# Optimization experiments

Hardware: AMD Instinct MI355X
Metric: run time of the kernel (lower is better)

The kernel has to match this reference:

```python
import jax, jax.numpy as jnp
import numpy as np

B, T, S = 4, 64, 256
E_ENC = 512   # encoder_hidden_size
D_DEC = 512   # decoder_hidden_size (must equal E_ENC per original math)
F_EMB = 128   # field_embed_size


def setup_inputs() -> dict:
    key = jax.random.key(0)
    ks = jax.random.split(key, 11)
    s = 0.05
    return {
        "output": jax.random.normal(ks[0], (B, T, D_DEC), jnp.float32),
        "encoder_hidden": jax.random.normal(ks[1], (S, B, E_ENC), jnp.float32),
        "input_z": jax.random.normal(ks[2], (B, S, F_EMB), jnp.float32),
        "W1": jax.random.normal(ks[3], (D_DEC, E_ENC), jnp.float32) * s,
        "b1": jnp.zeros((D_DEC,), jnp.float32),
        "W2": jax.random.normal(ks[4], (D_DEC, D_DEC), jnp.float32) * s,
        "b2": jnp.zeros((D_DEC,), jnp.float32),
        "W3": jax.random.normal(ks[5], (D_DEC, F_EMB), jnp.float32) * s,
        "b3": jnp.zeros((D_DEC,), jnp.float32),
        "W4": jax.random.normal(ks[6], (D_DEC, D_DEC), jnp.float32) * s,
        "b4": jnp.zeros((D_DEC,), jnp.float32),
    }


def reference(output, encoder_hidden, input_z, W1, b1, W2, b2, W3, b3, W4, b4):
    # out_hs: tanh(lin1(encoder_hidden)) on [S,B,D], then .view -> reshape to [B,S,D]
    out_hs = jnp.tanh(jnp.einsum('sbe,de->sbd', encoder_hidden, W1) + b1)
    out_hs = out_hs.reshape(out_hs.shape[1], out_hs.shape[0], out_hs.shape[2])  # [B,S,D] (raw view, as in torch)
    enc_r = encoder_hidden.reshape(encoder_hidden.shape[1], encoder_hidden.shape[0], encoder_hidden.shape[2])  # [B,S,E]

    out_fds = jnp.tanh(jnp.einsum('bsf,df->bsd', input_z, W3) + b3)   # [B,S,D]
    out2 = jnp.tanh(jnp.einsum('btd,ed->bte', output, W2) + b2)       # [B,T,D]
    out3 = jnp.tanh(jnp.einsum('btd,ed->bte', output, W4) + b4)       # [B,T,D]

    # Multiplicative gates, vectorized over decoder timesteps t: [B,T,S,D]
    g1 = out_hs[:, None, :, :] * out2[:, :, None, :]
    alpha = jax.nn.softmax(g1, axis=2)   # softmax over encoder positions S
    g2 = out_fds[:, None, :, :] * out3[:, :, None, :]
    beta = jax.nn.softmax(g2, axis=2)

    q = alpha * beta
    qn = jax.lax.stop_gradient(jnp.sum(q, axis=2, keepdims=True))  # .detach() in torch
    gamma = q / qn

    attn = jnp.sum(gamma * enc_r[:, None, :, :], axis=2)           # [B,T,D]
    concat = jnp.concatenate([output, attn], axis=-1)              # [B,T,2D]
    return concat, attn
```

## Files before the change

kernel.cpp:

```cpp
#include <hip/hip_runtime.h>

#define BB 4
#define TT 64
#define SS 256
#define DD 512
#define FEMB 128

typedef __attribute__((ext_vector_type(8))) short short8;
typedef __attribute__((ext_vector_type(4))) float floatx4;

__device__ __forceinline__ float fast_tanh(float x) {
    x = fminf(fmaxf(x, -10.f), 10.f);
    float t = __expf(2.f * x);
    return (t - 1.f) / (t + 1.f);
}

__device__ __forceinline__ unsigned int pack_bf2(float a, float b) {
    union { float f; unsigned int u; } ca, cb;
    ca.f = a; cb.f = b;
    unsigned int ua = ca.u + 0x7FFF + ((ca.u >> 16) & 1);
    unsigned int ub = cb.u + 0x7FFF + ((cb.u >> 16) & 1);
    return (ua >> 16) | (ub & 0xFFFF0000u);
}

__global__ __launch_bounds__(256) void cvt_kernel(
    const float* __restrict__ X, const float* __restrict__ Z, const float* __restrict__ Y,
    const float* __restrict__ W1, const float* __restrict__ W2,
    const float* __restrict__ W3, const float* __restrict__ W4,
    unsigned short* __restrict__ Xb, unsigned short* __restrict__ Zb,
    unsigned short* __restrict__ Yb, unsigned short* __restrict__ W1b,
    unsigned short* __restrict__ W2b, unsigned short* __restrict__ W3b,
    unsigned short* __restrict__ W4b)
{
    const int e = (blockIdx.x * 256 + threadIdx.x) * 4;
    const float* src; unsigned short* dst; int off;
    if (e < 524288)       { src = X;  dst = Xb;  off = 0; }
    else if (e < 655360)  { src = Z;  dst = Zb;  off = 524288; }
    else if (e < 786432)  { src = Y;  dst = Yb;  off = 655360; }
    else if (e < 1048576) { src = W1; dst = W1b; off = 786432; }
    else if (e < 1310720) { src = W2; dst = W2b; off = 1048576; }
    else if (e < 1376256) { src = W3; dst = W3b; off = 1310720; }
    else                  { src = W4; dst = W4b; off = 1376256; }
    const int i = e - off;
    float4 v = *(const float4*)&src[i];
    uint2 p;
    p.x = pack_bf2(v.x, v.y);
    p.y = pack_bf2(v.z, v.w);
    *(uint2*)&dst[i] = p;
}

__global__ __launch_bounds__(256) void gemm_mfma_kernel(
    const unsigned short* __restrict__ Xb, const unsigned short* __restrict__ Zb,
    const unsigned short* __restrict__ Yb,
    const unsigned short* __restrict__ W1b, const unsigned short* __restrict__ W2b,
    const unsigned short* __restrict__ W3b, const unsigned short* __restrict__ W4b,
    const float* __restrict__ b1, const float* __restrict__ b2,
    const float* __restrict__ b3, const float* __restrict__ b4,
    float* __restrict__ H, float* __restrict__ Fo,
    float* __restrict__ O2, float* __restrict__ O3)
{
    int id = blockIdx.x;
    const unsigned short* A; const unsigned short* W; const float* bias; float* C; int K;
    if (id < 128)      { A = Xb; W = W1b; bias = b1; C = H;  K = 512; }
    else if (id < 256) { id -= 128; A = Zb; W = W3b; bias = b3; C = Fo; K = 128; }
    else if (id < 288) { id -= 256; A = Yb; W = W2b; bias = b2; C = O2; K = 512; }
    else               { id -= 288; A = Yb; W = W4b; bias = b4; C = O3; K = 512; }
    const int m0 = (id >> 3) * 64;
    const int n0 = (id & 7) * 64;
    const int wv   = threadIdx.x >> 6;
    const int lane = threadIdx.x & 63;
    const int fr   = lane & 15;
    const int kh   = (lane >> 4) * 8;

    const unsigned short* Ap = A + (m0 + wv * 16 + fr) * K + kh;
    const unsigned short* Wp = W + (n0 + fr) * K + kh;
    const int WS = 16 * K;

    floatx4 acc0 = {0.f,0.f,0.f,0.f}, acc1 = acc0, acc2 = acc0, acc3 = acc0;

    short8 a  = *(const short8*)Ap;
    short8 w0 = *(const short8*)(Wp);
    short8 w1 = *(const short8*)(Wp + WS);
    short8 w2 = *(const short8*)(Wp + 2 * WS);
    short8 w3 = *(const short8*)(Wp + 3 * WS);

    for (int k0 = 0; k0 < K; k0 += 32) {
        const int kn = (k0 + 32 < K) ? (k0 + 32) : 0;
        short8 an  = *(const short8*)(Ap + kn);
        short8 wn0 = *(const short8*)(Wp + kn);
        short8 wn1 = *(const short8*)(Wp + WS + kn);
        short8 wn2 = *(const short8*)(Wp + 2 * WS + kn);
        short8 wn3 = *(const short8*)(Wp + 3 * WS + kn);
        acc0 = __builtin_amdgcn_mfma_f32_16x16x32_bf16(a, w0, acc0, 0, 0, 0);
        acc1 = __builtin_amdgcn_mfma_f32_16x16x32_bf16(a, w1, acc1, 0, 0, 0);
        acc2 = __builtin_amdgcn_mfma_f32_16x16x32_bf16(a, w2, acc2, 0, 0, 0);
        acc3 = __builtin_amdgcn_mfma_f32_16x16x32_bf16(a, w3, acc3, 0, 0, 0);
        a = an; w0 = wn0; w1 = wn1; w2 = wn2; w3 = wn3;
    }

    const int orow  = m0 + wv * 16 + (lane >> 4) * 4;
    const int ocol0 = n0 + fr;
    const float bv0 = bias[ocol0], bv1 = bias[ocol0 + 16],
                bv2 = bias[ocol0 + 32], bv3 = bias[ocol0 + 48];
    #pragma unroll
    for (int r = 0; r < 4; ++r) {
        float* Cr = C + (orow + r) * DD + ocol0;
        Cr[0]  = fast_tanh(acc0[r] + bv0);
        Cr[16] = fast_tanh(acc1[r] + bv1);
        Cr[32] = fast_tanh(acc2[r] + bv2);
        Cr[48] = fast_tanh(acc3[r] + bv3);
    }
}

__global__ __launch_bounds__(512) void attn_kernel(
    const float* __restrict__ H, const float* __restrict__ Fo,
    const float* __restrict__ X,
    const float* __restrict__ O2, const float* __restrict__ O3,
    const float* __restrict__ Y,
    float* __restrict__ out)
{
    const int idx = blockIdx.x;
    const int b   = (idx & 7) >> 1;
    const int rem = ((idx >> 3) << 1) | (idx & 1);
    const int t0  = (rem >> 2) * 2;
    const int dq  = rem & 3;
    const int tid = threadIdx.x;
    const int dl  = tid & 127;
    const int d   = dq * 128 + dl;
    const int sq  = tid >> 7;

    const int bt0 = b * TT + t0;
    const float u0 = O2[bt0 * DD + d],       v0 = O3[bt0 * DD + d];
    const float u1 = O2[(bt0 + 1) * DD + d], v1 = O3[(bt0 + 1) * DD + d];

    float l0 = 0.f, l1 = 0.f, a0 = 0.f, a1 = 0.f;
    const int base = (b * SS + sq * 64) * DD + d;
    const float* Hb = H  + base;
    const float* Fb = Fo + base;
    const float* Eb = X  + base;

    for (int s0 = 0; s0 < 64; s0 += 8) {
        float h[8], f[8], e[8];
        #pragma unroll
        for (int s = 0; s < 8; ++s) h[s] = Hb[(s0 + s) * DD];
        #pragma unroll
        for (int s = 0; s < 8; ++s) f[s] = Fb[(s0 + s) * DD];
        #pragma unroll
        for (int s = 0; s < 8; ++s) e[s] = Eb[(s0 + s) * DD];
        #pragma unroll
        for (int s = 0; s < 8; ++s) {
            const float w0 = fmaf(h[s], u0, f[s] * v0);
            const float x0 = __expf(w0);
            l0 += x0; a0 = fmaf(x0, e[s], a0);
            const float w1 = fmaf(h[s], u1, f[s] * v1);
            const float x1 = __expf(w1);
            l1 += x1; a1 = fmaf(x1, e[s], a1);
        }
    }

    __shared__ float red[3][128][9];
    if (sq) {
        red[sq-1][dl][0] = l0; red[sq-1][dl][1] = l1;
        red[sq-1][dl][2] = a0; red[sq-1][dl][3] = a1;
    }
    __syncthreads();
    if (sq == 0) {
        #pragma unroll
        for (int q = 0; q < 3; ++q) {
            l0 += red[q][dl][0]; l1 += red[q][dl][1];
            a0 += red[q][dl][2]; a1 += red[q][dl][3];
        }
        const float r0 = a0 / l0, r1 = a1 / l1;
        out[BB * TT * 2 * DD + bt0 * DD + d]       = r0;
        out[BB * TT * 2 * DD + (bt0 + 1) * DD + d] = r1;
        out[bt0 * 2 * DD + DD + d]                 = r0;
        out[(bt0 + 1) * 2 * DD + DD + d]           = r1;
        out[bt0 * 2 * DD + d]                      = Y[bt0 * DD + d];
        out[(bt0 + 1) * 2 * DD + d]                = Y[(bt0 + 1) * DD + d];
    }
}

extern "C" void kernel_launch(void* const* d_in, const int* in_sizes, int n_in,
                              void* d_out, int out_size, void* d_ws, size_t ws_size,
                              hipStream_t stream)
{
    const float* Y  = (const float*)d_in[0];
    const float* X  = (const float*)d_in[1];
    const float* Z  = (const float*)d_in[2];
    const float* W1 = (const float*)d_in[3];
    const float* b1 = (const float*)d_in[4];
    const float* W2 = (const float*)d_in[5];
    const float* b2 = (const float*)d_in[6];
    const float* W3 = (const float*)d_in[7];
    const float* b3 = (const float*)d_in[8];
    const float* W4 = (const float*)d_in[9];
    const float* b4 = (const float*)d_in[10];
    float* out = (float*)d_out;

    float* H  = (float*)d_ws;
    float* Fo = H  + 1024 * 512;
    float* O2 = Fo + 1024 * 512;
    float* O3 = O2 + 256 * 512;
    unsigned short* Xb  = (unsigned short*)(O3 + 256 * 512);
    unsigned short* Zb  = Xb  + 524288;
    unsigned short* Yb  = Zb  + 131072;
    unsigned short* W1b = Yb  + 131072;
    unsigned short* W2b = W1b + 262144;
    unsigned short* W3b = W2b + 262144;
    unsigned short* W4b = W3b + 65536;

    cvt_kernel<<<1600, 256, 0, stream>>>(X, Z, Y, W1, W2, W3, W4,
                                         Xb, Zb, Yb, W1b, W2b, W3b, W4b);
    gemm_mfma_kernel<<<320, 256, 0, stream>>>(Xb, Zb, Yb, W1b, W2b, W3b, W4b,
                                              b1, b2, b3, b4, H, Fo, O2, O3);
    attn_kernel<<<512, 512, 0, stream>>>(H, Fo, X, O2, O3, Y, out);
}
```

Measured before the change: 110.3 us.

## Fuse conversion, GEMMs and attention into one persistent kernel with grid barrier

```diff
diff --git a/kernel.cpp b/kernel.cpp
--- a/kernel.cpp
+++ b/kernel.cpp
@@ -4,7 +4,6 @@
 #define TT 64
 #define SS 256
 #define DD 512
-#define FEMB 128
 
 typedef __attribute__((ext_vector_type(8))) short short8;
 typedef __attribute__((ext_vector_type(4))) float floatx4;
@@ -15,168 +14,198 @@
     return (t - 1.f) / (t + 1.f);
 }
 
-__device__ __forceinline__ unsigned int pack_bf2(float a, float b) {
-    union { float f; unsigned int u; } ca, cb;
-    ca.f = a; cb.f = b;
-    unsigned int ua = ca.u + 0x7FFF + ((ca.u >> 16) & 1);
-    unsigned int ub = cb.u + 0x7FFF + ((cb.u >> 16) & 1);
-    return (ua >> 16) | (ub & 0xFFFF0000u);
-}
-
-__global__ __launch_bounds__(256) void cvt_kernel(
-    const float* __restrict__ X, const float* __restrict__ Z, const float* __restrict__ Y,
-    const float* __restrict__ W1, const float* __restrict__ W2,
-    const float* __restrict__ W3, const float* __restrict__ W4,
-    unsigned short* __restrict__ Xb, unsigned short* __restrict__ Zb,
-    unsigned short* __restrict__ Yb, unsigned short* __restrict__ W1b,
-    unsigned short* __restrict__ W2b, unsigned short* __restrict__ W3b,
-    unsigned short* __restrict__ W4b)
+__device__ __forceinline__ unsigned int cvt_pk_bf16(float lo, float hi) {
+    unsigned int r;
+    asm("v_cvt_pk_bf16_f32 %0, %1, %2" : "=v"(r) : "v"(lo), "v"(hi));
+    return r;
+}
+
+__device__ __forceinline__ short8 load_cvt8(const float* __restrict__ p) {
+    floatx4 lo = *(const floatx4*)p;
+    floatx4 hi = *(const floatx4*)(p + 4);
+    union { short8 s; unsigned int u[4]; } r;
+    r.u[0] = cvt_pk_bf16(lo[0], lo[1]);
+    r.u[1] = cvt_pk_bf16(lo[2], lo[3]);
+    r.u[2] = cvt_pk_bf16(hi[0], hi[1]);
+    r.u[3] = cvt_pk_bf16(hi[2], hi[3]);
+    return r.s;
+}
+
+template<int NF>
+__device__ __forceinline__ void gemm_tile(
+    const float* __restrict__ A, const float* __restrict__ W,
+    const float* __restrict__ bias, float* __restrict__ C,
+    const int K, const int m0, const int n0)
 {
-    const int e = (blockIdx.x * 256 + threadIdx.x) * 4;
-    const float* src; unsigned short* dst; int off;
-    if (e < 524288)       { src = X;  dst = Xb;  off = 0; }
-    else if (e < 655360)  { src = Z;  dst = Zb;  off = 524288; }
-    else if (e < 786432)  { src = Y;  dst = Yb;  off = 655360; }
-    else if (e < 1048576) { src = W1; dst = W1b; off = 786432; }
-    else if (e < 1310720) { src = W2; dst = W2b; off = 1048576; }
-    else if (e < 1376256) { src = W3; dst = W3b; off = 1310720; }
-    else                  { src = W4; dst = W4b; off = 1376256; }
-    const int i = e - off;
-    float4 v = *(const float4*)&src[i];
-    uint2 p;
-    p.x = pack_bf2(v.x, v.y);
-    p.y = pack_bf2(v.z, v.w);
-    *(uint2*)&dst[i] = p;
-}
-
-__global__ __launch_bounds__(256) void gemm_mfma_kernel(
-    const unsigned short* __restrict__ Xb, const unsigned short* __restrict__ Zb,
-    const unsigned short* __restrict__ Yb,
-    const unsigned short* __restrict__ W1b, const unsigned short* __restrict__ W2b,
-    const unsigned short* __restrict__ W3b, const unsigned short* __restrict__ W4b,
-    const float* __restrict__ b1, const float* __restrict__ b2,
-    const float* __restrict__ b3, const float* __restrict__ b4,
-    float* __restrict__ H, float* __restrict__ Fo,
-    float* __restrict__ O2, float* __restrict__ O3)
-{
-    int id = blockIdx.x;
-    const unsigned short* A; const unsigned short* W; const float* bias; float* C; int K;
-    if (id < 128)      { A = Xb; W = W1b; bias = b1; C = H;  K = 512; }
-    else if (id < 256) { id -= 128; A = Zb; W = W3b; bias = b3; C = Fo; K = 128; }
-    else if (id < 288) { id -= 256; A = Yb; W = W2b; bias = b2; C = O2; K = 512; }
-    else               { id -= 288; A = Yb; W = W4b; bias = b4; C = O3; K = 512; }
-    const int m0 = (id >> 3) * 64;
-    const int n0 = (id & 7) * 64;
     const int wv   = threadIdx.x >> 6;
     const int lane = threadIdx.x & 63;
     const int fr   = lane & 15;
     const int kh   = (lane >> 4) * 8;
 
-    const unsigned short* Ap = A + (m0 + wv * 16 + fr) * K + kh;
-    const unsigned short* Wp = W + (n0 + fr) * K + kh;
+    const float* Ap = A + (m0 + wv * 16 + fr) * K + kh;
+    const float* Wp = W + (n0 + fr) * K + kh;
     const int WS = 16 * K;
 
     floatx4 acc0 = {0.f,0.f,0.f,0.f}, acc1 = acc0, acc2 = acc0, acc3 = acc0;
 
-    short8 a  = *(const short8*)Ap;
-    short8 w0 = *(const short8*)(Wp);
-    short8 w1 = *(const short8*)(Wp + WS);
-    short8 w2 = *(const short8*)(Wp + 2 * WS);
-    short8 w3 = *(const short8*)(Wp + 3 * WS);
+    short8 a  = load_cvt8(Ap);
+    short8 w0 = load_cvt8(Wp);
+    short8 w1 = load_cvt8(Wp + WS);
+    short8 w2, w3;
+    if constexpr (NF == 4) { w2 = load_cvt8(Wp + 2 * WS); w3 = load_cvt8(Wp + 3 * WS); }
 
     for (int k0 = 0; k0 < K; k0 += 32) {
         const int kn = (k0 + 32 < K) ? (k0 + 32) : 0;
-        short8 an  = *(const short8*)(Ap + kn);
-        short8 wn0 = *(const short8*)(Wp + kn);
-        short8 wn1 = *(const short8*)(Wp + WS + kn);
-        short8 wn2 = *(const short8*)(Wp + 2 * WS + kn);
-        short8 wn3 = *(const short8*)(Wp + 3 * WS + kn);
+        short8 an  = load_cvt8(Ap + kn);
+        short8 wn0 = load_cvt8(Wp + kn);
+        short8 wn1 = load_cvt8(Wp + WS + kn);
+        short8 wn2, wn3;
+        if constexpr (NF == 4) { wn2 = load_cvt8(Wp + 2 * WS + kn); wn3 = load_cvt8(Wp + 3 * WS + kn); }
         acc0 = __builtin_amdgcn_mfma_f32_16x16x32_bf16(a, w0, acc0, 0, 0, 0);
         acc1 = __builtin_amdgcn_mfma_f32_16x16x32_bf16(a, w1, acc1, 0, 0, 0);
-        acc2 = __builtin_amdgcn_mfma_f32_16x16x32_bf16(a, w2, acc2, 0, 0, 0);
-        acc3 = __builtin_amdgcn_mfma_f32_16x16x32_bf16(a, w3, acc3, 0, 0, 0);
-        a = an; w0 = wn0; w1 = wn1; w2 = wn2; w3 = wn3;
-    }
-
-    const int orow  = m0 + wv * 16 + (lane >> 4) * 4;
-    const int ocol0 = n0 + fr;
-    const float bv0 = bias[ocol0], bv1 = bias[ocol0 + 16],
-                bv2 = bias[ocol0 + 32], bv3 = bias[ocol0 + 48];
+        if constexpr (NF == 4) {
+            acc2 = __builtin_amdgcn_mfma_f32_16x16x32_bf16(a, w2, acc2, 0, 0, 0);
+            acc3 = __builtin_amdgcn_mfma_f32_16x16x32_bf16(a, w3, acc3, 0, 0, 0);
+        }
+        a = an; w0 = wn0; w1 = wn1;
+        if constexpr (NF == 4) { w2 = wn2; w3 = wn3; }
+    }
+
+    const int orow = m0 + wv * 16 + (lane >> 4) * 4;
+    const int oc0  = n0 + fr;
+    const float bv0 = bias[oc0], bv1 = bias[oc0 + 16];
+    float bv2 = 0.f, bv3 = 0.f;
+    if constexpr (NF == 4) { bv2 = bias[oc0 + 32]; bv3 = bias[oc0 + 48]; }
     #pragma unroll
     for (int r = 0; r < 4; ++r) {
-        float* Cr = C + (orow + r) * DD + ocol0;
+        float* Cr = C + (orow + r) * DD + oc0;
         Cr[0]  = fast_tanh(acc0[r] + bv0);
         Cr[16] = fast_tanh(acc1[r] + bv1);
-        Cr[32] = fast_tanh(acc2[r] + bv2);
-        Cr[48] = fast_tanh(acc3[r] + bv3);
-    }
-}
-
-__global__ __launch_bounds__(512) void attn_kernel(
-    const float* __restrict__ H, const float* __restrict__ Fo,
-    const float* __restrict__ X,
-    const float* __restrict__ O2, const float* __restrict__ O3,
-    const float* __restrict__ Y,
-    float* __restrict__ out)
+        if constexpr (NF == 4) {
+            Cr[32] = fast_tanh(acc2[r] + bv2);
+            Cr[48] = fast_tanh(acc3[r] + bv3);
+        }
+    }
+}
+
+__device__ __forceinline__ void grid_barrier(int* __restrict__ bar, const int target) {
+    __syncthreads();
+    if (threadIdx.x == 0) {
+        __threadfence();
+        __hip_atomic_fetch_add(bar, 1, __ATOMIC_ACQ_REL, __HIP_MEMORY_SCOPE_AGENT);
+        int spins = 0;
+        while (__hip_atomic_load(bar, __ATOMIC_RELAXED, __HIP_MEMORY_SCOPE_AGENT) < target) {
+            __builtin_amdgcn_s_sleep(2);
+            if (++spins > (1 << 22)) break;
+        }
+        __threadfence();
+    }
+    __syncthreads();
+}
+
+__global__ __launch_bounds__(256, 2) void fused_kernel(
+    const float* __restrict__ X,  const float* __restrict__ Z,  const float* __restrict__ Y,
+    const float* __restrict__ W1, const float* __restrict__ b1,
+    const float* __restrict__ W2, const float* __restrict__ b2,
+    const float* __restrict__ W3, const float* __restrict__ b3,
+    const float* __restrict__ W4, const float* __restrict__ b4,
+    float* __restrict__ H, float* __restrict__ Fo,
+    float* __restrict__ O2, float* __restrict__ O3,
+    int* __restrict__ bar, float* __restrict__ out)
 {
-    const int idx = blockIdx.x;
-    const int b   = (idx & 7) >> 1;
-    const int rem = ((idx >> 3) << 1) | (idx & 1);
-    const int t0  = (rem >> 2) * 2;
-    const int dq  = rem & 3;
-    const int tid = threadIdx.x;
-    const int dl  = tid & 127;
-    const int d   = dq * 128 + dl;
-    const int sq  = tid >> 7;
-
-    const int bt0 = b * TT + t0;
-    const float u0 = O2[bt0 * DD + d],       v0 = O3[bt0 * DD + d];
-    const float u1 = O2[(bt0 + 1) * DD + d], v1 = O3[(bt0 + 1) * DD + d];
-
-    float l0 = 0.f, l1 = 0.f, a0 = 0.f, a1 = 0.f;
-    const int base = (b * SS + sq * 64) * DD + d;
-    const float* Hb = H  + base;
-    const float* Fb = Fo + base;
-    const float* Eb = X  + base;
-
-    for (int s0 = 0; s0 < 64; s0 += 8) {
-        float h[8], f[8], e[8];
-        #pragma unroll
-        for (int s = 0; s < 8; ++s) h[s] = Hb[(s0 + s) * DD];
-        #pragma unroll
-        for (int s = 0; s < 8; ++s) f[s] = Fb[(s0 + s) * DD];
-        #pragma unroll
-        for (int s = 0; s < 8; ++s) e[s] = Eb[(s0 + s) * DD];
-        #pragma unroll
-        for (int s = 0; s < 8; ++s) {
-            const float w0 = fmaf(h[s], u0, f[s] * v0);
-            const float x0 = __expf(w0);
-            l0 += x0; a0 = fmaf(x0, e[s], a0);
-            const float w1 = fmaf(h[s], u1, f[s] * v1);
-            const float x1 = __expf(w1);
-            l1 += x1; a1 = fmaf(x1, e[s], a1);
-        }
-    }
-
-    __shared__ float red[3][128][9];
-    if (sq) {
-        red[sq-1][dl][0] = l0; red[sq-1][dl][1] = l1;
-        red[sq-1][dl][2] = a0; red[sq-1][dl][3] = a1;
-    }
-    __syncthreads();
-    if (sq == 0) {
-        #pragma unroll
-        for (int q = 0; q < 3; ++q) {
-            l0 += red[q][dl][0]; l1 += red[q][dl][1];
-            a0 += red[q][dl][2]; a1 += red[q][dl][3];
-        }
-        const float r0 = a0 / l0, r1 = a1 / l1;
-        out[BB * TT * 2 * DD + bt0 * DD + d]       = r0;
-        out[BB * TT * 2 * DD + (bt0 + 1) * DD + d] = r1;
-        out[bt0 * 2 * DD + DD + d]                 = r0;
-        out[(bt0 + 1) * 2 * DD + DD + d]           = r1;
-        out[bt0 * 2 * DD + d]                      = Y[bt0 * DD + d];
-        out[(bt0 + 1) * 2 * DD + d]                = Y[(bt0 + 1) * DD + d];
+    {
+        const int id = blockIdx.x;
+        if (id < 256) {
+            gemm_tile<2>(X, W1, b1, H, 512, (id >> 4) * 64, (id & 15) * 32);
+        } else if (id < 384) {
+            const int q = id - 256;
+            gemm_tile<4>(Z, W3, b3, Fo, 128, (q >> 3) * 64, (q & 7) * 64);
+        } else if (id < 448) {
+            const int q = id - 384;
+            gemm_tile<2>(Y, W2, b2, O2, 512, (q >> 4) * 64, (q & 15) * 32);
+        } else {
+            const int q = id - 448;
+            gemm_tile<2>(Y, W4, b4, O3, 512, (q >> 4) * 64, (q & 15) * 32);
+        }
+    }
+
+    grid_barrier(bar, 512);
+
+    {
+        const int idx = blockIdx.x;
+        const int b   = (idx & 7) >> 1;
+        const int rem = ((idx >> 3) << 1) | (idx & 1);
+        const int t0  = (rem >> 2) * 2;
+        const int dq  = rem & 3;
+        const int tid = threadIdx.x;
+        const int dv  = tid & 31;
+        const int sg  = tid >> 5;
+        const int d   = dq * 128 + dv * 4;
+        const int bt0 = b * TT + t0;
+
+        const floatx4 u0 = *(const floatx4*)&O2[bt0 * DD + d];
+        const floatx4 v0 = *(const floatx4*)&O3[bt0 * DD + d];
+        const floatx4 u1 = *(const floatx4*)&O2[(bt0 + 1) * DD + d];
+        const floatx4 v1 = *(const floatx4*)&O3[(bt0 + 1) * DD + d];
+
+        floatx4 l0 = {0.f,0.f,0.f,0.f}, l1 = l0, a0 = l0, a1 = l0;
+        const int base = (b * SS + sg * 32) * DD + d;
+        const float* Hb = H  + base;
+        const float* Fb = Fo + base;
+        const float* Eb = X  + base;
+
+        for (int s0 = 0; s0 < 32; s0 += 4) {
+            floatx4 h[4], f[4], e[4];
+            #pragma unroll
+            for (int s = 0; s < 4; ++s) h[s] = *(const floatx4*)&Hb[(s0 + s) * DD];
+            #pragma unroll
+            for (int s = 0; s < 4; ++s) f[s] = *(const floatx4*)&Fb[(s0 + s) * DD];
+            #pragma unroll
+            for (int s = 0; s < 4; ++s) e[s] = *(const floatx4*)&Eb[(s0 + s) * DD];
+            #pragma unroll
+            for (int s = 0; s < 4; ++s) {
+                const floatx4 w0 = h[s] * u0 + f[s] * v0;
+                const floatx4 w1 = h[s] * u1 + f[s] * v1;
+                floatx4 x0, x1;
+                #pragma unroll
+                for (int j = 0; j < 4; ++j) { x0[j] = __expf(w0[j]); x1[j] = __expf(w1[j]); }
+                l0 += x0; a0 += x0 * e[s];
+                l1 += x1; a1 += x1 * e[s];
+            }
+        }
+
+        __shared__ float red[7][16][32];
+        if (sg != 0) {
+            #pragma unroll
+            for (int j = 0; j < 4; ++j) {
+                red[sg - 1][j][dv]      = l0[j];
+                red[sg - 1][4 + j][dv]  = l1[j];
+                red[sg - 1][8 + j][dv]  = a0[j];
+                red[sg - 1][12 + j][dv] = a1[j];
+            }
+        }
+        __syncthreads();
+        if (sg == 0) {
+            #pragma unroll
+            for (int q = 0; q < 7; ++q) {
+                #pragma unroll
+                for (int j = 0; j < 4; ++j) {
+                    l0[j] += red[q][j][dv];
+                    l1[j] += red[q][4 + j][dv];
+                    a0[j] += red[q][8 + j][dv];
+                    a1[j] += red[q][12 + j][dv];
+                }
+            }
+            const floatx4 r0 = a0 / l0;
+            const floatx4 r1 = a1 / l1;
+            const int OFFA = BB * TT * 2 * DD;
+            *(floatx4*)&out[OFFA + bt0 * DD + d]       = r0;
+            *(floatx4*)&out[OFFA + (bt0 + 1) * DD + d] = r1;
+            *(floatx4*)&out[bt0 * 2 * DD + DD + d]       = r0;
+            *(floatx4*)&out[(bt0 + 1) * 2 * DD + DD + d] = r1;
+            *(floatx4*)&out[bt0 * 2 * DD + d]       = *(const floatx4*)&Y[bt0 * DD + d];
+            *(floatx4*)&out[(bt0 + 1) * 2 * DD + d] = *(const floatx4*)&Y[(bt0 + 1) * DD + d];
+        }
     }
 }
 
@@ -197,21 +226,13 @@
     const float* b4 = (const float*)d_in[10];
     float* out = (float*)d_out;
 
-    float* H  = (float*)d_ws;
-    float* Fo = H  + 1024 * 512;
-    float* O2 = Fo + 1024 * 512;
-    float* O3 = O2 + 256 * 512;
-    unsigned short* Xb  = (unsigned short*)(O3 + 256 * 512);
-    unsigned short* Zb  = Xb  + 524288;
-    unsigned short* Yb  = Zb  + 131072;
-    unsigned short* W1b = Yb  + 131072;
-    unsigned short* W2b = W1b + 262144;
-    unsigned short* W3b = W2b + 262144;
-    unsigned short* W4b = W3b + 65536;
-
-    cvt_kernel<<<1600, 256, 0, stream>>>(X, Z, Y, W1, W2, W3, W4,
-                                         Xb, Zb, Yb, W1b, W2b, W3b, W4b);
-    gemm_mfma_kernel<<<320, 256, 0, stream>>>(Xb, Zb, Yb, W1b, W2b, W3b, W4b,
-                                              b1, b2, b3, b4, H, Fo, O2, O3);
-    attn_kernel<<<512, 512, 0, stream>>>(H, Fo, X, O2, O3, Y, out);
-}
+    int*   bar = (int*)d_ws;
+    float* H   = (float*)d_ws + 64;
+    float* Fo  = H  + 1024 * 512;
+    float* O2  = Fo + 1024 * 512;
+    float* O3  = O2 + 256 * 512;
+
+    hipMemsetAsync(bar, 0, 256, stream);
+    fused_kernel<<<512, 256, 0, stream>>>(X, Z, Y, W1, b1, W2, b2, W3, b3, W4, b4,
+                                          H, Fo, O2, O3, bar, out);
+}
```

New measurement: 170.8 us. 1.55x slower.
